# Optimization experiments

Measured on AMD Instinct MI355X. Metric: run time of the kernel, lower is better.

The kernel has to match this reference:

```python
import jax, jax.numpy as jnp
import numpy as np

EMBED = 1024
HEADS = 16
HEAD_DIM = EMBED // HEADS


def setup_inputs() -> dict:
    key = jax.random.key(0)
    ks = jax.random.split(key, 8)
    N, S = 4, 2048
    inp = {
        "values": jax.random.normal(ks[0], (N, S, EMBED), dtype=jnp.float32),
        "keys": jax.random.normal(ks[1], (N, S, EMBED), dtype=jnp.float32),
        "queries": jax.random.normal(ks[2], (N, S, EMBED), dtype=jnp.float32),
        # Linear weights stored as [in, out] (torch Linear applies x @ W.T; here W already transposed)
        "W_v": jax.random.normal(ks[3], (EMBED, EMBED), dtype=jnp.float32) / np.sqrt(EMBED),
        "W_k": jax.random.normal(ks[4], (EMBED, EMBED), dtype=jnp.float32) / np.sqrt(EMBED),
        "W_q": jax.random.normal(ks[5], (EMBED, EMBED), dtype=jnp.float32) / np.sqrt(EMBED),
        "W_o": jax.random.normal(ks[6], (EMBED, EMBED), dtype=jnp.float32) / np.sqrt(EMBED),
        "b_o": jax.random.normal(ks[7], (EMBED,), dtype=jnp.float32) * 0.01,
    }
    return inp


def reference(values, keys, queries, W_v, W_k, W_q, W_o, b_o):
    N, q_len, _ = queries.shape
    v = (values @ W_v).reshape(N, -1, HEADS, HEAD_DIM)   # [n, v_len, h, d]
    k = (keys @ W_k).reshape(N, -1, HEADS, HEAD_DIM)     # [n, k_len, h, d]
    q = (queries @ W_q).reshape(N, -1, HEADS, HEAD_DIM)  # [n, q_len, h, d]
    # NOTE: original scales by sqrt(embed_size), not sqrt(head_dim)
    energy = jnp.einsum('nqhd,nkhd->nhqk', q, k) / jnp.sqrt(jnp.float32(EMBED))
    attn = jax.nn.softmax(energy, axis=-1)
    out = jnp.einsum('nhqk,nkhd->nqhd', attn, v).reshape(N, q_len, EMBED)
    return out @ W_o + b_o
```

## Files before the change

### kernel.cpp

```cpp
#include <hip/hip_runtime.h>
#include <hip/hip_bf16.h>
#include <stdint.h>

typedef __attribute__((ext_vector_type(8))) short short8;
typedef __attribute__((ext_vector_type(4))) float f32x4;
typedef __attribute__((ext_vector_type(4))) unsigned short u16x4;
typedef unsigned short u16;

#define EMBED 1024
#define SEQ 2048
#define NBATCH 4
#define MROWS (NBATCH * SEQ)

__device__ __forceinline__ u16 f2bf(float f) {
  union { float f; uint32_t u; } v; v.f = f;
  uint32_t r = v.u + 0x7fffu + ((v.u >> 16) & 1u);
  return (u16)(r >> 16);
}

__device__ __forceinline__ uint32_t cvtpk(float lo, float hi) {
  uint32_t r;
  asm("v_cvt_pk_bf16_f32 %0, %1, %2" : "=v"(r) : "v"(lo), "v"(hi));
  return r;
}

__device__ __forceinline__ float vexp2(float x) {
  float r;
  asm("v_exp_f32 %0, %1" : "=v"(r) : "v"(x));
  return r;
}

__device__ __forceinline__ void gld16(const void* g, void* l) {
  __builtin_amdgcn_global_load_lds((const __attribute__((address_space(1))) void*)g,
                                   (__attribute__((address_space(3))) void*)l, 16, 0, 0);
}

__global__ __launch_bounds__(256) void prep_kernel(const float4* __restrict__ a,
                                                   const float4* __restrict__ b,
                                                   const float4* __restrict__ c,
                                                   u16x4* __restrict__ oa,
                                                   u16x4* __restrict__ ob,
                                                   u16x4* __restrict__ oc, int n4,
                                                   const float* __restrict__ W0,
                                                   const float* __restrict__ W1,
                                                   const float* __restrict__ W2,
                                                   const float* __restrict__ W3,
                                                   u16* __restrict__ T0,
                                                   u16* __restrict__ T1,
                                                   u16* __restrict__ T2,
                                                   u16* __restrict__ T3) {
  if (blockIdx.x < 1536) {
    int which = blockIdx.x >> 9;
    const float4* in = which == 0 ? a : (which == 1 ? b : c);
    u16x4* out = which == 0 ? oa : (which == 1 ? ob : oc);
    int stride = 512 * 256;
    for (int i = (blockIdx.x & 511) * 256 + threadIdx.x; i < n4; i += stride) {
      float4 v = in[i];
      u16x4 o = { f2bf(v.x), f2bf(v.y), f2bf(v.z), f2bf(v.w) };
      out[i] = o;
    }
  } else {
    int id = blockIdx.x - 1536;
    int z = id >> 10;
    const float* W = z == 0 ? W0 : (z == 1 ? W1 : (z == 2 ? W2 : W3));
    u16* Wt = z == 0 ? T0 : (z == 1 ? T1 : (z == 2 ? T2 : T3));
    __shared__ float tile[32][33];
    int bx = (id & 31) * 32, by = ((id >> 5) & 31) * 32;
    int tx = threadIdx.x & 31, ty = threadIdx.x >> 5;
#pragma unroll
    for (int i = 0; i < 32; i += 8)
      tile[ty + i][tx] = W[(size_t)(by + ty + i) * EMBED + bx + tx];
    __syncthreads();
#pragma unroll
    for (int i = 0; i < 32; i += 8)
      Wt[(size_t)(bx + ty + i) * EMBED + by + tx] = f2bf(tile[tx][ty + i]);
  }
}

template <bool DYN>
__device__ __forceinline__ void gemm_body(const u16* __restrict__ A,
                                          const u16* __restrict__ Bt,
                                          void* __restrict__ outp,
                                          const float* __restrict__ bias,
                                          float oscale, int epi) {
  constexpr int K = 1024;
  __shared__ u16 lsA[128 * 64];
  __shared__ u16 lsB[128 * 64];
  const int t = threadIdx.x, l = t & 63, w = t >> 6;
  const int g = l >> 4, r15 = l & 15;
  const int m0 = blockIdx.y * 128, n0 = blockIdx.x * 128;
  const int wm = (w >> 1) * 64, wn = (w & 1) * 64;
  f32x4 acc[4][4] = {};
  const int srow = t >> 3;
  const int sc16 = (t & 7) * 16;

  const u16* Ap[4]; const u16* Bp[4];
#pragma unroll
  for (int j = 0; j < 4; ++j) {
    int row = srow + j * 32;
    int colswz = (sc16 ^ ((row & 7) << 4)) >> 1;
    Ap[j] = A  + (size_t)(m0 + row) * K + colswz;
    Bp[j] = Bt + (size_t)(n0 + row) * K + colswz;
  }

  for (int k0 = 0; k0 < K; k0 += 64) {
#pragma unroll
    for (int j = 0; j < 4; ++j) {
      gld16(Ap[j] + k0, lsA + j * 2048 + w * 512);
      gld16(Bp[j] + k0, lsB + j * 2048 + w * 512);
    }
    __syncthreads();
    short8 af[2][4], bfv[2][4];
#pragma unroll
    for (int kk = 0; kk < 2; ++kk) {
#pragma unroll
      for (int mi = 0; mi < 4; ++mi) {
        int row = wm + mi * 16 + r15;
        af[kk][mi] = *(const short8*)((const char*)lsA + row * 128 + ((kk * 64 + g * 16) ^ ((row & 7) << 4)));
      }
#pragma unroll
      for (int ni = 0; ni < 4; ++ni) {
        int row = wn + ni * 16 + r15;
        bfv[kk][ni] = *(const short8*)((const char*)lsB + row * 128 + ((kk * 64 + g * 16) ^ ((row & 7) << 4)));
      }
    }
#pragma unroll
    for (int kk = 0; kk < 2; ++kk)
#pragma unroll
      for (int mi = 0; mi < 4; ++mi)
#pragma unroll
        for (int ni = 0; ni < 4; ++ni)
          acc[mi][ni] = __builtin_amdgcn_mfma_f32_16x16x32_bf16(af[kk][mi], bfv[kk][ni], acc[mi][ni], 0, 0, 0);
    __syncthreads();
  }

#pragma unroll
  for (int mi = 0; mi < 4; ++mi)
#pragma unroll
    for (int ni = 0; ni < 4; ++ni)
#pragma unroll
      for (int r = 0; r < 4; ++r) {
        int row = m0 + wm + mi * 16 + g * 4 + r;
        int col = n0 + wn + ni * 16 + r15;
        float v = acc[mi][ni][r];
        if (DYN) {
          if (epi == 0) {
            ((u16*)outp)[(((size_t)(row >> 11) * 16 + (col >> 6)) * SEQ + (row & 2047)) * 64 + (col & 63)] = f2bf(v * oscale);
          } else {
            ((u16*)outp)[(((size_t)(row >> 11) * 16 + (col >> 6)) * 64 + (col & 63)) * SEQ + (row & 2047)] = f2bf(v);
          }
        } else {
          ((float*)outp)[(size_t)row * EMBED + col] = v + bias[col];
        }
      }
}

__global__ __launch_bounds__(256) void qkv_gemm(const u16* __restrict__ Xq,
                                                const u16* __restrict__ Xk,
                                                const u16* __restrict__ Xv,
                                                const u16* __restrict__ Wqt,
                                                const u16* __restrict__ Wkt,
                                                const u16* __restrict__ Wvt,
                                                u16* __restrict__ Qb,
                                                u16* __restrict__ Kb,
                                                u16* __restrict__ Vtb,
                                                float qscale) {
  int z = blockIdx.z;
  const u16* A  = z == 0 ? Xq : (z == 1 ? Xk : Xv);
  const u16* Bt = z == 0 ? Wqt : (z == 1 ? Wkt : Wvt);
  u16* out      = z == 0 ? Qb : (z == 1 ? Kb : Vtb);
  gemm_body<true>(A, Bt, out, nullptr, z == 0 ? qscale : 1.0f, z == 2 ? 1 : 0);
}

__global__ __launch_bounds__(256) void gemm_o(const u16* __restrict__ A,
                                              const u16* __restrict__ Bt,
                                              float* __restrict__ outp,
                                              const float* __restrict__ bias) {
  gemm_body<false>(A, Bt, outp, bias, 1.0f, 2);
}

__global__ __launch_bounds__(256) void attn_kernel(const u16* __restrict__ Q,
                                                   const u16* __restrict__ Kb,
                                                   const u16* __restrict__ Vt,
                                                   u16* __restrict__ AO) {
  __shared__ u16 lsK[2][64 * 64];
  __shared__ u16 lsV[2][64 * 64];
  const int t = threadIdx.x, l = t & 63, w = t >> 6;
  const int g = l >> 4, r15 = l & 15;

  const int flat = blockIdx.x;
  const int work = (flat & 7) * 128 + (flat >> 3);
  const int bh = work >> 4;
  const int q0 = (work & 15) * 128;

  const u16* Qh = Q + (size_t)bh * SEQ * 64;
  const u16* Kh = Kb + (size_t)bh * SEQ * 64;
  const u16* Vh = Vt + (size_t)bh * 64 * SEQ;

  short8 qf[2][2];
#pragma unroll
  for (int qi = 0; qi < 2; ++qi)
#pragma unroll
    for (int dh = 0; dh < 2; ++dh)
      qf[qi][dh] = *(const short8*)&Qh[(size_t)(q0 + w * 32 + qi * 16 + r15) * 64 + dh * 32 + g * 8];

  const short8 kones = { 0x3F80, 0x3F80, 0x3F80, 0x3F80, 0x3F80, 0x3F80, 0x3F80, 0x3F80 };
  f32x4 ssum[2] = {};
  f32x4 oacc[4][2] = {};

  const int srow = t >> 3;
  const int scolb = (t & 7) * 16;

  uint4 vreg[2];

  auto STAGE_K = [&](int buf, int kv0) {
#pragma unroll
    for (int j = 0; j < 2; ++j) {
      int row = j * 32 + srow;
      int colswz = (scolb ^ ((row & 7) << 4)) >> 1;
      gld16(Kh + (size_t)(kv0 + row) * 64 + colswz, &lsK[buf][j * 2048 + w * 512]);
    }
  };
  auto VLOAD = [&](int kv0) {
#pragma unroll
    for (int j = 0; j < 2; ++j) {
      int row = j * 32 + srow;
      vreg[j] = *(const uint4*)(Vh + (size_t)row * SEQ + kv0 + (scolb >> 1));
    }
  };
  auto VSTORE = [&](int buf) {
#pragma unroll
    for (int j = 0; j < 2; ++j) {
      int row = j * 32 + srow;
      int c4 = (row & 7) << 4, c3 = ((row >> 3) & 1) << 3;
      char* base = (char*)&lsV[buf][0] + row * 128 + (scolb ^ c4);
      *(uint2*)(base + c3)       = make_uint2(vreg[j].x, vreg[j].y);
      *(uint2*)(base + (8 ^ c3)) = make_uint2(vreg[j].z, vreg[j].w);
    }
  };

  auto STEP = [&](int buf, bool pre, int a) {
    if (pre) {
      VLOAD((a + 1) * 64);
      STAGE_K(buf ^ 1, (a + 1) * 64);
    }
    const u16* Kc = lsK[buf];
    const u16* Vc = lsV[buf];

    f32x4 sacc[2][4] = {};
    __builtin_amdgcn_s_setprio(1);
#pragma unroll
    for (int c = 0; c < 4; ++c) {
      int krow = c * 16 + r15;
      int sz = (krow & 7) << 4;
#pragma unroll
      for (int dh = 0; dh < 2; ++dh) {
        short8 kf = *(const short8*)((const char*)Kc + krow * 128 + ((dh * 64 + g * 16) ^ sz));
#pragma unroll
        for (int qi = 0; qi < 2; ++qi)
          sacc[qi][c] = __builtin_amdgcn_mfma_f32_16x16x32_bf16(kf, qf[qi][dh], sacc[qi][c], 0, 0, 0);
      }
    }
    __builtin_amdgcn_s_setprio(0);

    short8 pb[2][2];
#pragma unroll
    for (int qi = 0; qi < 2; ++qi) {
#pragma unroll
      for (int c = 0; c < 4; ++c)
#pragma unroll
        for (int r = 0; r < 4; ++r)
          sacc[qi][c][r] = vexp2(sacc[qi][c][r]);
#pragma unroll
      for (int kh = 0; kh < 2; ++kh) {
        union { uint32_t u[4]; short8 s; } pu;
        pu.u[0] = cvtpk(sacc[qi][2 * kh][0],     sacc[qi][2 * kh][1]);
        pu.u[1] = cvtpk(sacc[qi][2 * kh][2],     sacc[qi][2 * kh][3]);
        pu.u[2] = cvtpk(sacc[qi][2 * kh + 1][0], sacc[qi][2 * kh + 1][1]);
        pu.u[3] = cvtpk(sacc[qi][2 * kh + 1][2], sacc[qi][2 * kh + 1][3]);
        pb[qi][kh] = pu.s;
      }
    }

#pragma unroll
    for (int qi = 0; qi < 2; ++qi)
#pragma unroll
      for (int kh = 0; kh < 2; ++kh)
        ssum[qi] = __builtin_amdgcn_mfma_f32_16x16x32_bf16(kones, pb[qi][kh], ssum[qi], 0, 0, 0);

    __builtin_amdgcn_s_setprio(1);
#pragma unroll
    for (int dc = 0; dc < 4; ++dc) {
      int vrow = dc * 16 + r15;
      int sz = ((vrow & 7) << 4) | (((vrow >> 3) & 1) << 3);
      const char* vb = (const char*)Vc + vrow * 128;
#pragma unroll
      for (int kh = 0; kh < 2; ++kh) {
        union { uint2 v[2]; short8 s; } va;
        va.v[0] = *(const uint2*)(vb + ((kh * 64 + 8 * g) ^ sz));
        va.v[1] = *(const uint2*)(vb + ((kh * 64 + 32 + 8 * g) ^ sz));
#pragma unroll
        for (int qi = 0; qi < 2; ++qi)
          oacc[dc][qi] = __builtin_amdgcn_mfma_f32_16x16x32_bf16(va.s, pb[qi][kh], oacc[dc][qi], 0, 0, 0);
      }
    }
    __builtin_amdgcn_s_setprio(0);

    if (pre) VSTORE(buf ^ 1);
    __syncthreads();
  };

  VLOAD(0);
  STAGE_K(0, 0);
  VSTORE(0);
  __syncthreads();

#pragma unroll 1
  for (int pair = 0; pair < 16; ++pair) {
    STEP(0, true, 2 * pair);
    STEP(1, pair != 15, 2 * pair + 1);
  }

  const int nb = bh >> 4, h = bh & 15;
  float inv[2] = { 1.0f / ssum[0][0], 1.0f / ssum[1][0] };
#pragma unroll
  for (int dc = 0; dc < 4; ++dc)
#pragma unroll
    for (int qi = 0; qi < 2; ++qi) {
      int q = q0 + w * 32 + qi * 16 + r15;
      int d = dc * 16 + g * 4;
      uint32_t a = cvtpk(oacc[dc][qi][0] * inv[qi], oacc[dc][qi][1] * inv[qi]);
      uint32_t b = cvtpk(oacc[dc][qi][2] * inv[qi], oacc[dc][qi][3] * inv[qi]);
      uint2* dst = (uint2*)&AO[((size_t)(nb * SEQ + q)) * EMBED + h * 64 + d];
      *dst = make_uint2(a, b);
    }
}

extern "C" void kernel_launch(void* const* d_in, const int* in_sizes, int n_in,
                              void* d_out, int out_size, void* d_ws, size_t ws_size,
                              hipStream_t stream) {
  const float* values  = (const float*)d_in[0];
  const float* keys    = (const float*)d_in[1];
  const float* queries = (const float*)d_in[2];
  const float* W_v = (const float*)d_in[3];
  const float* W_k = (const float*)d_in[4];
  const float* W_q = (const float*)d_in[5];
  const float* W_o = (const float*)d_in[6];
  const float* b_o = (const float*)d_in[7];

  const size_t XSZ = (size_t)MROWS * EMBED;
  const size_t WSZ = (size_t)EMBED * EMBED;
  u16* ws = (u16*)d_ws;
  u16* Xv  = ws;
  u16* Xk  = ws + XSZ;
  u16* Xq  = ws + 2 * XSZ;
  u16* Wvt = ws + 3 * XSZ;
  u16* Wkt = Wvt + WSZ;
  u16* Wqt = Wkt + WSZ;
  u16* Wot = Wqt + WSZ;
  u16* Qb  = Wot + WSZ;
  u16* Kb  = Qb + XSZ;
  u16* Vtb = Kb + XSZ;
  u16* AO  = Xv;

  int n4 = (int)(XSZ / 4);
  prep_kernel<<<5632, 256, 0, stream>>>((const float4*)values, (const float4*)keys,
                                        (const float4*)queries,
                                        (u16x4*)Xv, (u16x4*)Xk, (u16x4*)Xq, n4,
                                        W_v, W_k, W_q, W_o, Wvt, Wkt, Wqt, Wot);

  const float QSCALE = 0.03125f * 1.4426950408889634f;
  dim3 gq(EMBED / 128, MROWS / 128, 3);
  qkv_gemm<<<gq, 256, 0, stream>>>(Xq, Xk, Xv, Wqt, Wkt, Wvt, Qb, Kb, Vtb, QSCALE);

  attn_kernel<<<1024, 256, 0, stream>>>(Qb, Kb, Vtb, AO);

  dim3 gg(EMBED / 128, MROWS / 128);
  gemm_o<<<gg, 256, 0, stream>>>(AO, Wot, (float*)d_out, b_o);
}
```

Baseline: 230.1 us.

## Fuse fp32-to-bf16 activation conversion into QKV GEMM operand loads

The separate prep pass that converted the three fp32 activation tensors to bf16 is removed. The QKV GEMM now streams fp32 A tiles straight into LDS with a swizzled layout and converts them to bf16 in registers before the MFMAs. This avoids writing and re-reading about 48MB of intermediate bf16 data. In exchange the GEMM loads twice the A bytes per tile, uses more LDS (32KB for A), and spends extra VALU work on conversion that is repeated across the 8 column blocks.

```diff
diff --git a/kernel.cpp b/kernel.cpp
--- a/kernel.cpp
+++ b/kernel.cpp
@@ -35,13 +35,7 @@
                                    (__attribute__((address_space(3))) void*)l, 16, 0, 0);
 }
 
-__global__ __launch_bounds__(256) void prep_kernel(const float4* __restrict__ a,
-                                                   const float4* __restrict__ b,
-                                                   const float4* __restrict__ c,
-                                                   u16x4* __restrict__ oa,
-                                                   u16x4* __restrict__ ob,
-                                                   u16x4* __restrict__ oc, int n4,
-                                                   const float* __restrict__ W0,
+__global__ __launch_bounds__(256) void prep_kernel(const float* __restrict__ W0,
                                                    const float* __restrict__ W1,
                                                    const float* __restrict__ W2,
                                                    const float* __restrict__ W3,
@@ -49,40 +43,132 @@
                                                    u16* __restrict__ T1,
                                                    u16* __restrict__ T2,
                                                    u16* __restrict__ T3) {
-  if (blockIdx.x < 1536) {
-    int which = blockIdx.x >> 9;
-    const float4* in = which == 0 ? a : (which == 1 ? b : c);
-    u16x4* out = which == 0 ? oa : (which == 1 ? ob : oc);
-    int stride = 512 * 256;
-    for (int i = (blockIdx.x & 511) * 256 + threadIdx.x; i < n4; i += stride) {
-      float4 v = in[i];
-      u16x4 o = { f2bf(v.x), f2bf(v.y), f2bf(v.z), f2bf(v.w) };
-      out[i] = o;
-    }
-  } else {
-    int id = blockIdx.x - 1536;
-    int z = id >> 10;
-    const float* W = z == 0 ? W0 : (z == 1 ? W1 : (z == 2 ? W2 : W3));
-    u16* Wt = z == 0 ? T0 : (z == 1 ? T1 : (z == 2 ? T2 : T3));
-    __shared__ float tile[32][33];
-    int bx = (id & 31) * 32, by = ((id >> 5) & 31) * 32;
-    int tx = threadIdx.x & 31, ty = threadIdx.x >> 5;
-#pragma unroll
-    for (int i = 0; i < 32; i += 8)
-      tile[ty + i][tx] = W[(size_t)(by + ty + i) * EMBED + bx + tx];
+  int id = blockIdx.x;
+  int z = id >> 10;
+  const float* W = z == 0 ? W0 : (z == 1 ? W1 : (z == 2 ? W2 : W3));
+  u16* Wt = z == 0 ? T0 : (z == 1 ? T1 : (z == 2 ? T2 : T3));
+  __shared__ float tile[32][33];
+  int bx = (id & 31) * 32, by = ((id >> 5) & 31) * 32;
+  int tx = threadIdx.x & 31, ty = threadIdx.x >> 5;
+#pragma unroll
+  for (int i = 0; i < 32; i += 8)
+    tile[ty + i][tx] = W[(size_t)(by + ty + i) * EMBED + bx + tx];
+  __syncthreads();
+#pragma unroll
+  for (int i = 0; i < 32; i += 8)
+    Wt[(size_t)(bx + ty + i) * EMBED + by + tx] = f2bf(tile[tx][ty + i]);
+}
+
+__global__ __launch_bounds__(256) void qkv_gemm(const float* __restrict__ Aq,
+                                                const float* __restrict__ Ak,
+                                                const float* __restrict__ Av,
+                                                const u16* __restrict__ Wqt,
+                                                const u16* __restrict__ Wkt,
+                                                const u16* __restrict__ Wvt,
+                                                u16* __restrict__ Qb,
+                                                u16* __restrict__ Kb,
+                                                u16* __restrict__ Vtb,
+                                                float qscale) {
+  constexpr int K = 1024;
+  __shared__ float lsAf[128 * 64];
+  __shared__ u16 lsB[128 * 64];
+  const int z = blockIdx.z;
+  const float* A = z == 0 ? Aq : (z == 1 ? Ak : Av);
+  const u16* Bt  = z == 0 ? Wqt : (z == 1 ? Wkt : Wvt);
+  u16* outp      = z == 0 ? Qb : (z == 1 ? Kb : Vtb);
+  const float oscale = z == 0 ? qscale : 1.0f;
+  const int epi = (z == 2) ? 1 : 0;
+
+  const int t = threadIdx.x, l = t & 63, w = t >> 6;
+  const int g = l >> 4, r15 = l & 15;
+  const int m0 = blockIdx.y * 128, n0 = blockIdx.x * 128;
+  const int wm = (w >> 1) * 64, wn = (w & 1) * 64;
+  f32x4 acc[4][4] = {};
+
+  const int srow = t >> 3;
+  const int sc16 = (t & 7) * 16;
+  const u16* Bp[4];
+#pragma unroll
+  for (int j = 0; j < 4; ++j) {
+    int row = srow + j * 32;
+    int colswz = (sc16 ^ ((row & 7) << 4)) >> 1;
+    Bp[j] = Bt + (size_t)(n0 + row) * K + colswz;
+  }
+
+  const int arow_b = t >> 4;
+  const int au = t & 15;
+  const float* Apf[8];
+#pragma unroll
+  for (int j = 0; j < 8; ++j) {
+    int row = j * 16 + arow_b;
+    int s = ((row & 7) << 1) | ((row >> 3) & 1);
+    Apf[j] = A + (size_t)(m0 + row) * K + (au ^ s) * 4;
+  }
+
+  for (int k0 = 0; k0 < K; k0 += 64) {
+#pragma unroll
+    for (int j = 0; j < 4; ++j)
+      gld16(Bp[j] + k0, lsB + j * 2048 + w * 512);
+#pragma unroll
+    for (int j = 0; j < 8; ++j)
+      gld16(Apf[j] + k0, (char*)lsAf + j * 4096 + w * 1024);
     __syncthreads();
-#pragma unroll
-    for (int i = 0; i < 32; i += 8)
-      Wt[(size_t)(bx + ty + i) * EMBED + by + tx] = f2bf(tile[tx][ty + i]);
-  }
-}
-
-template <bool DYN>
-__device__ __forceinline__ void gemm_body(const u16* __restrict__ A,
-                                          const u16* __restrict__ Bt,
-                                          void* __restrict__ outp,
-                                          const float* __restrict__ bias,
-                                          float oscale, int epi) {
+
+    short8 af[2][4], bfv[2][4];
+#pragma unroll
+    for (int kk = 0; kk < 2; ++kk) {
+#pragma unroll
+      for (int mi = 0; mi < 4; ++mi) {
+        int row = wm + mi * 16 + r15;
+        int s = ((row & 7) << 1) | ((row >> 3) & 1);
+        int v = kk * 8 + g * 2;
+        const char* base = (const char*)lsAf + row * 256;
+        f32x4 a0 = *(const f32x4*)(base + ((v ^ s) * 16));
+        f32x4 a1 = *(const f32x4*)(base + (((v + 1) ^ s) * 16));
+        union { uint32_t u[4]; short8 sv; } pu;
+        pu.u[0] = cvtpk(a0[0], a0[1]);
+        pu.u[1] = cvtpk(a0[2], a0[3]);
+        pu.u[2] = cvtpk(a1[0], a1[1]);
+        pu.u[3] = cvtpk(a1[2], a1[3]);
+        af[kk][mi] = pu.sv;
+      }
+#pragma unroll
+      for (int ni = 0; ni < 4; ++ni) {
+        int row = wn + ni * 16 + r15;
+        bfv[kk][ni] = *(const short8*)((const char*)lsB + row * 128 + ((kk * 64 + g * 16) ^ ((row & 7) << 4)));
+      }
+    }
+#pragma unroll
+    for (int kk = 0; kk < 2; ++kk)
+#pragma unroll
+      for (int mi = 0; mi < 4; ++mi)
+#pragma unroll
+        for (int ni = 0; ni < 4; ++ni)
+          acc[mi][ni] = __builtin_amdgcn_mfma_f32_16x16x32_bf16(af[kk][mi], bfv[kk][ni], acc[mi][ni], 0, 0, 0);
+    __syncthreads();
+  }
+
+#pragma unroll
+  for (int mi = 0; mi < 4; ++mi)
+#pragma unroll
+    for (int ni = 0; ni < 4; ++ni)
+#pragma unroll
+      for (int r = 0; r < 4; ++r) {
+        int row = m0 + wm + mi * 16 + g * 4 + r;
+        int col = n0 + wn + ni * 16 + r15;
+        float v = acc[mi][ni][r];
+        if (epi == 0) {
+          ((u16*)outp)[(((size_t)(row >> 11) * 16 + (col >> 6)) * SEQ + (row & 2047)) * 64 + (col & 63)] = f2bf(v * oscale);
+        } else {
+          ((u16*)outp)[(((size_t)(row >> 11) * 16 + (col >> 6)) * 64 + (col & 63)) * SEQ + (row & 2047)] = f2bf(v);
+        }
+      }
+}
+
+__global__ __launch_bounds__(256) void gemm_o(const u16* __restrict__ A,
+                                              const u16* __restrict__ Bt,
+                                              float* __restrict__ outp,
+                                              const float* __restrict__ bias) {
   constexpr int K = 1024;
   __shared__ u16 lsA[128 * 64];
   __shared__ u16 lsB[128 * 64];
@@ -142,41 +228,8 @@
       for (int r = 0; r < 4; ++r) {
         int row = m0 + wm + mi * 16 + g * 4 + r;
         int col = n0 + wn + ni * 16 + r15;
-        float v = acc[mi][ni][r];
-        if (DYN) {
-          if (epi == 0) {
-            ((u16*)outp)[(((size_t)(row >> 11) * 16 + (col >> 6)) * SEQ + (row & 2047)) * 64 + (col & 63)] = f2bf(v * oscale);
-          } else {
-            ((u16*)outp)[(((size_t)(row >> 11) * 16 + (col >> 6)) * 64 + (col & 63)) * SEQ + (row & 2047)] = f2bf(v);
-          }
-        } else {
-          ((float*)outp)[(size_t)row * EMBED + col] = v + bias[col];
-        }
-      }
-}
-
-__global__ __launch_bounds__(256) void qkv_gemm(const u16* __restrict__ Xq,
-                                                const u16* __restrict__ Xk,
-                                                const u16* __restrict__ Xv,
-                                                const u16* __restrict__ Wqt,
-                                                const u16* __restrict__ Wkt,
-                                                const u16* __restrict__ Wvt,
-                                                u16* __restrict__ Qb,
-                                                u16* __restrict__ Kb,
-                                                u16* __restrict__ Vtb,
-                                                float qscale) {
-  int z = blockIdx.z;
-  const u16* A  = z == 0 ? Xq : (z == 1 ? Xk : Xv);
-  const u16* Bt = z == 0 ? Wqt : (z == 1 ? Wkt : Wvt);
-  u16* out      = z == 0 ? Qb : (z == 1 ? Kb : Vtb);
-  gemm_body<true>(A, Bt, out, nullptr, z == 0 ? qscale : 1.0f, z == 2 ? 1 : 0);
-}
-
-__global__ __launch_bounds__(256) void gemm_o(const u16* __restrict__ A,
-                                              const u16* __restrict__ Bt,
-                                              float* __restrict__ outp,
-                                              const float* __restrict__ bias) {
-  gemm_body<false>(A, Bt, outp, bias, 1.0f, 2);
+        outp[(size_t)row * EMBED + col] = acc[mi][ni][r] + bias[col];
+      }
 }
 
 __global__ __launch_bounds__(256) void attn_kernel(const u16* __restrict__ Q,
@@ -281,7 +334,6 @@
         pb[qi][kh] = pu.s;
       }
     }
-
 #pragma unroll
     for (int qi = 0; qi < 2; ++qi)
 #pragma unroll
@@ -351,27 +403,20 @@
   const size_t XSZ = (size_t)MROWS * EMBED;
   const size_t WSZ = (size_t)EMBED * EMBED;
   u16* ws = (u16*)d_ws;
-  u16* Xv  = ws;
-  u16* Xk  = ws + XSZ;
-  u16* Xq  = ws + 2 * XSZ;
-  u16* Wvt = ws + 3 * XSZ;
+  u16* Wvt = ws;
   u16* Wkt = Wvt + WSZ;
   u16* Wqt = Wkt + WSZ;
   u16* Wot = Wqt + WSZ;
   u16* Qb  = Wot + WSZ;
   u16* Kb  = Qb + XSZ;
   u16* Vtb = Kb + XSZ;
-  u16* AO  = Xv;
-
-  int n4 = (int)(XSZ / 4);
-  prep_kernel<<<5632, 256, 0, stream>>>((const float4*)values, (const float4*)keys,
-                                        (const float4*)queries,
-                                        (u16x4*)Xv, (u16x4*)Xk, (u16x4*)Xq, n4,
-                                        W_v, W_k, W_q, W_o, Wvt, Wkt, Wqt, Wot);
+  u16* AO  = Vtb + XSZ;
+
+  prep_kernel<<<4096, 256, 0, stream>>>(W_v, W_k, W_q, W_o, Wvt, Wkt, Wqt, Wot);
 
   const float QSCALE = 0.03125f * 1.4426950408889634f;
   dim3 gq(EMBED / 128, MROWS / 128, 3);
-  qkv_gemm<<<gq, 256, 0, stream>>>(Xq, Xk, Xv, Wqt, Wkt, Wvt, Qb, Kb, Vtb, QSCALE);
+  qkv_gemm<<<gq, 256, 0, stream>>>(queries, keys, values, Wqt, Wkt, Wvt, Qb, Kb, Vtb, QSCALE);
 
   attn_kernel<<<1024, 256, 0, stream>>>(Qb, Kb, Vtb, AO);
 
```

New measurement: 257.7 us. 12.0% more time.
